# Performance work log

Measured on AMD Instinct MI355X. Metric: run time of the kernel, lower is better.

## Reference

```python
import jax, jax.numpy as jnp
from jax import lax
import numpy as np

P = 0.25  # dropouto


def _lstm(x, Wih, Whh, b):
    """Standard torch-layout LSTM over [B, T, I]; gate order i,f,g,o.
    Wih: [4H, I], Whh: [4H, H], b: [4H] (= b_ih + b_hh). Returns [B, T, H]."""
    B, T, I = x.shape
    H = Whh.shape[1]
    # Precompute input contributions for all timesteps in one GEMM.
    xg = jnp.einsum('bti,gi->btg', x, Wih) + b  # [B, T, 4H]
    xg = jnp.swapaxes(xg, 0, 1)  # [T, B, 4H]

    def step(carry, xt):
        h, c = carry
        g = xt + h @ Whh.T  # [B, 4H]
        i, f, gg, o = jnp.split(g, 4, axis=-1)
        i = jax.nn.sigmoid(i)
        f = jax.nn.sigmoid(f)
        gg = jnp.tanh(gg)
        o = jax.nn.sigmoid(o)
        c = f * c + i * gg
        h = o * jnp.tanh(c)
        return (h, c), h

    h0 = jnp.zeros((B, H), x.dtype)
    c0 = jnp.zeros((B, H), x.dtype)
    _, hs = lax.scan(step, (h0, c0), xg)  # hs: [T, B, H]
    return jnp.swapaxes(hs, 0, 1)


def setup_inputs() -> dict:
    key = jax.random.key(0)
    ks = jax.random.split(key, 10)
    B, T = 512, 4096
    H1, H2 = 16, 1
    s = 0.25  # small init scale
    x = jax.random.normal(ks[0], (B, T, 1), jnp.float32)
    Wih1 = jax.random.normal(ks[1], (4 * H1, 1), jnp.float32) * s
    Whh1 = jax.random.normal(ks[2], (4 * H1, H1), jnp.float32) * s
    b1 = jax.random.normal(ks[3], (4 * H1,), jnp.float32) * s
    Wih2 = jax.random.normal(ks[4], (4 * H2, H1), jnp.float32) * s
    Whh2 = jax.random.normal(ks[5], (4 * H2, H2), jnp.float32) * s
    b2 = jax.random.normal(ks[6], (4 * H2,), jnp.float32) * s
    keep = 1.0 - P
    # Variational dropout masks: one mask per sequence, shared over time.
    mask1 = jax.random.bernoulli(ks[7], keep, (B, 1, H1)).astype(jnp.float32) / keep
    mask2 = jax.random.bernoulli(ks[8], keep, (B, 1, H2)).astype(jnp.float32) / keep
    return {"x": x, "Wih1": Wih1, "Whh1": Whh1, "b1": b1,
            "Wih2": Wih2, "Whh2": Whh2, "b2": b2,
            "mask1": mask1, "mask2": mask2}


def reference(x, Wih1, Whh1, b1, Wih2, Whh2, b2, mask1, mask2):
    out = _lstm(x, Wih1, Whh1, b1) * mask1   # dropouto on lstm1 output
    out = _lstm(out, Wih2, Whh2, b2) * mask2  # dropouto on lstm2 output
    return out  # [B, T, 1]
```

## Files before the change

kernel.cpp:

```cpp
#include <hip/hip_runtime.h>

typedef __fp16 f16x2 __attribute__((ext_vector_type(2)));
typedef unsigned u32x2 __attribute__((ext_vector_type(2)));

static __device__ __forceinline__ float rdlane(float v, int l) {
  return __uint_as_float(__builtin_amdgcn_readlane(__float_as_uint(v), (unsigned)l));
}
static __device__ __forceinline__ unsigned rdlane_u(unsigned v, int l) {
  return __builtin_amdgcn_readlane(v, (unsigned)l);
}

template <int CTRL>
static __device__ __forceinline__ float qperm(float v) {
  return __uint_as_float(__builtin_amdgcn_update_dpp(
      0u, __float_as_uint(v), CTRL, 0xF, 0xF, true));
}

static __device__ __forceinline__ float xswap_hi(float v) {
#if __has_builtin(__builtin_amdgcn_permlane32_swap)
  u32x2 r = __builtin_amdgcn_permlane32_swap(
      __float_as_uint(v), __float_as_uint(v), false, false);
  return __uint_as_float(r.y);
#else
  float a = v, b;
  asm("v_mov_b32 %0, %1\n\t"
      "s_nop 1\n\t"
      "v_permlane32_swap_b32 %1, %0"
      : "=&v"(b), "+v"(a));
  return b;
#endif
}

static __device__ __forceinline__ float exp2a(float x) {
  float r;
  asm("v_exp_f32 %0, %1" : "=v"(r) : "v"(x));
  return r;
}
static __device__ __forceinline__ float rcpa(float x) {
  return __builtin_amdgcn_rcpf(x);
}

static __device__ __forceinline__ float dot2f(f16x2 a, unsigned bu, float c) {
#if __has_builtin(__builtin_amdgcn_fdot2)
  return __builtin_amdgcn_fdot2(a, __builtin_bit_cast(f16x2, bu), c, false);
#else
  float r = c;
  f16x2 b = __builtin_bit_cast(f16x2, bu);
  asm("v_dot2_f32_f16 %0, %1, %2, %0" : "+v"(r) : "v"(a), "v"(b));
  return r;
#endif
}

#define QP_XOR1 0xB1
#define QP_XOR2 0x4E
#define QP_XOR3 0x1B
#define QP_BC3  0xFF

__global__ __launch_bounds__(64, 1) void vdd_lstm_kernel(
    const float* __restrict__ x,
    const float* __restrict__ Wih1,
    const float* __restrict__ Whh1,
    const float* __restrict__ b1,
    const float* __restrict__ Wih2,
    const float* __restrict__ Whh2,
    const float* __restrict__ b2,
    const float* __restrict__ mask1,
    const float* __restrict__ mask2,
    float* __restrict__ out,
    int T) {
  const int b = blockIdx.x;
  const int lane = threadIdx.x;
  const int j = lane >> 2;
  const int gt = lane & 3;
  const int row = gt * 16 + j;

  const float LOG2E = 1.4426950408889634f;
  const bool isg = (gt == 2);
  const float sc = isg ? (-2.f * LOG2E) : (-LOG2E);
  const float aA = isg ? (-4.f * LOG2E) : 1.f;
  const float aC = isg ? (2.f * LOG2E) : 0.f;
  const bool isl1 = (lane == 1);

  f16x2 wh1[8];
#pragma unroll
  for (int m = 0; m < 8; ++m) {
    wh1[m].x = (__fp16)(Whh1[row * 16 + m] * sc);
    wh1[m].y = (__fp16)(Whh1[row * 16 + m + 8] * sc);
  }
  f16x2 wh2[8];
#pragma unroll
  for (int m = 0; m < 8; ++m) {
    wh2[m].x = (__fp16)(Wih2[gt * 16 + m] * mask1[b * 16 + m] * sc);
    wh2[m].y = (__fp16)(Wih2[gt * 16 + m + 8] * mask1[b * 16 + m + 8] * sc);
  }
  const float wih1 = Wih1[row] * sc;
  const float bb1  = b1[row] * sc;
  const float whh2 = Whh2[gt] * sc;
  const float bb2  = b2[gt] * sc;
  const float m2   = mask2[b];

  const float* xb = x + (size_t)b * T;
  float* ob = out + (size_t)b * T;

  float h, cs;
  float cs2p = 0.f;
  float o2p = 0.f;
  float och = 0.f;

  const int NCH = T >> 6;
  const int tmax = T - 1;

  {
    float pre = __fmaf_rn(wih1, xb[0], bb1);
    float a1 = __fmaf_rn(aA, rcpa(1.f + exp2a(pre)), aC);
    float g1 = qperm<QP_XOR2>(a1);
    float o1 = qperm<QP_XOR3>(a1);
    cs = a1 * g1;
    float th = __fmaf_rn(2.f, rcpa(1.f + exp2a(cs)), -1.f);
    h = o1 * th;
  }

  auto body = [&](float sx, bool doSel, int slot) {
    float hhi = xswap_hi(h);
    f16x2 tp = __builtin_bit_cast(
        f16x2, __builtin_amdgcn_cvt_pkrtz(h, hhi));
    unsigned tpu = __builtin_bit_cast(unsigned, tp);
    unsigned sp[8];
#pragma unroll
    for (int m = 0; m < 8; ++m) sp[m] = rdlane_u(tpu, 4 * m);

    float accA = __fmaf_rn(wih1, sx, bb1);
    float accB = dot2f(wh1[1], sp[1], 0.f);
    accA = dot2f(wh1[0], sp[0], accA);
    accB = dot2f(wh1[3], sp[3], accB);
    accA = dot2f(wh1[2], sp[2], accA);
    accB = dot2f(wh1[5], sp[5], accB);
    accA = dot2f(wh1[4], sp[4], accA);
    accB = dot2f(wh1[7], sp[7], accB);
    accA = dot2f(wh1[6], sp[6], accA);
    float pre = accA + accB;

    float accC = dot2f(wh2[0], sp[0], bb2);
    float accD = dot2f(wh2[1], sp[1], 0.f);
    accC = dot2f(wh2[2], sp[2], accC);
    accD = dot2f(wh2[3], sp[3], accD);
    accC = dot2f(wh2[4], sp[4], accC);
    accD = dot2f(wh2[5], sp[5], accD);
    accC = dot2f(wh2[6], sp[6], accC);
    accD = dot2f(wh2[7], sp[7], accD);
    float d2 = accC + accD;

    float a1 = __fmaf_rn(aA, rcpa(1.f + exp2a(pre)), aC);
    float f1 = qperm<QP_XOR1>(a1);
    float g1 = qperm<QP_XOR2>(a1);
    float o1 = qperm<QP_XOR3>(a1);
    cs = __fmaf_rn(f1, cs, a1 * g1);

    float z = isl1 ? cs2p : cs;
    float thv = __fmaf_rn(2.f, rcpa(1.f + exp2a(z)), -1.f);
    float hn = o1 * thv;
    float th2 = rdlane(thv, 1);
    float h2b = o2p * th2;

    float pre2 = __fmaf_rn(whh2, h2b, d2);
    float a2 = __fmaf_rn(aA, rcpa(1.f + exp2a(pre2)), aC);
    float i2l = qperm<QP_XOR1>(a2);
    float g2l = qperm<QP_XOR3>(a2);
    cs2p = __fmaf_rn(a2, cs2p, i2l * g2l);
    o2p = qperm<QP_BC3>(a2);

    float ov = h2b * m2;
    if (doSel) och = (lane == slot) ? ov : och;
    h = hn;
  };

  int idx0 = 2 + lane;
  idx0 = idx0 > tmax ? tmax : idx0;
  float w = xb[idx0];

  body(xb[1], false, 0);

  for (int ch = 0; ch < NCH; ++ch) {
    int idxn = (ch + 1) * 64 + 2 + lane;
    idxn = idxn > tmax ? tmax : idxn;
    float wn = xb[idxn];

#pragma unroll 16
    for (int s2 = 0; s2 < 64; ++s2) {
      float sx = rdlane(w, s2);
      body(sx, true, s2);
    }

    ob[(ch << 6) + lane] = och;
    w = wn;
  }
}

extern "C" void kernel_launch(void* const* d_in, const int* in_sizes, int n_in,
                              void* d_out, int out_size, void* d_ws, size_t ws_size,
                              hipStream_t stream) {
  const float* x     = (const float*)d_in[0];
  const float* Wih1  = (const float*)d_in[1];
  const float* Whh1  = (const float*)d_in[2];
  const float* b1    = (const float*)d_in[3];
  const float* Wih2  = (const float*)d_in[4];
  const float* Whh2  = (const float*)d_in[5];
  const float* b2    = (const float*)d_in[6];
  const float* mask1 = (const float*)d_in[7];
  const float* mask2 = (const float*)d_in[8];
  float* out = (float*)d_out;

  const int B = in_sizes[8];
  const int T = in_sizes[0] / B;

  vdd_lstm_kernel<<<dim3(B), dim3(64), 0, stream>>>(
      x, Wih1, Whh1, b1, Wih2, Whh2, b2, mask1, mask2, out, T);
}
```

Baseline: 540.1 us.

## Split LSTM layers into producer/consumer wavefronts pipelined through LDS

```diff
diff --git a/kernel.cpp b/kernel.cpp
--- a/kernel.cpp
+++ b/kernel.cpp
@@ -56,7 +56,10 @@
 #define QP_XOR3 0x1B
 #define QP_BC3  0xFF
 
-__global__ __launch_bounds__(64, 1) void vdd_lstm_kernel(
+#define SLOT_W 65
+#define BUF_W  (64 * SLOT_W)
+
+__global__ __launch_bounds__(128, 1) void vdd_lstm_kernel(
     const float* __restrict__ x,
     const float* __restrict__ Wih1,
     const float* __restrict__ Whh1,
@@ -68,8 +71,12 @@
     const float* __restrict__ mask2,
     float* __restrict__ out,
     int T) {
+  __shared__ unsigned lds_u[2 * BUF_W];
+
   const int b = blockIdx.x;
-  const int lane = threadIdx.x;
+  const int tid = threadIdx.x;
+  const bool isA = tid < 64;
+  const int lane = tid & 63;
   const int j = lane >> 2;
   const int gt = lane & 3;
   const int row = gt * 16 + j;
@@ -81,118 +88,133 @@
   const float aC = isg ? (2.f * LOG2E) : 0.f;
   const bool isl1 = (lane == 1);
 
-  f16x2 wh1[8];
-#pragma unroll
-  for (int m = 0; m < 8; ++m) {
-    wh1[m].x = (__fp16)(Whh1[row * 16 + m] * sc);
-    wh1[m].y = (__fp16)(Whh1[row * 16 + m + 8] * sc);
-  }
-  f16x2 wh2[8];
-#pragma unroll
-  for (int m = 0; m < 8; ++m) {
-    wh2[m].x = (__fp16)(Wih2[gt * 16 + m] * mask1[b * 16 + m] * sc);
-    wh2[m].y = (__fp16)(Wih2[gt * 16 + m + 8] * mask1[b * 16 + m + 8] * sc);
-  }
-  const float wih1 = Wih1[row] * sc;
-  const float bb1  = b1[row] * sc;
-  const float whh2 = Whh2[gt] * sc;
-  const float bb2  = b2[gt] * sc;
-  const float m2   = mask2[b];
-
   const float* xb = x + (size_t)b * T;
   float* ob = out + (size_t)b * T;
-
-  float h, cs;
-  float cs2p = 0.f;
-  float o2p = 0.f;
-  float och = 0.f;
-
   const int NCH = T >> 6;
   const int tmax = T - 1;
 
-  {
-    float pre = __fmaf_rn(wih1, xb[0], bb1);
-    float a1 = __fmaf_rn(aA, rcpa(1.f + exp2a(pre)), aC);
-    float g1 = qperm<QP_XOR2>(a1);
-    float o1 = qperm<QP_XOR3>(a1);
-    cs = a1 * g1;
-    float th = __fmaf_rn(2.f, rcpa(1.f + exp2a(cs)), -1.f);
-    h = o1 * th;
-  }
-
-  auto body = [&](float sx, bool doSel, int slot) {
-    float hhi = xswap_hi(h);
-    f16x2 tp = __builtin_bit_cast(
-        f16x2, __builtin_amdgcn_cvt_pkrtz(h, hhi));
-    unsigned tpu = __builtin_bit_cast(unsigned, tp);
-    unsigned sp[8];
-#pragma unroll
-    for (int m = 0; m < 8; ++m) sp[m] = rdlane_u(tpu, 4 * m);
-
-    float accA = __fmaf_rn(wih1, sx, bb1);
-    float accB = dot2f(wh1[1], sp[1], 0.f);
-    accA = dot2f(wh1[0], sp[0], accA);
-    accB = dot2f(wh1[3], sp[3], accB);
-    accA = dot2f(wh1[2], sp[2], accA);
-    accB = dot2f(wh1[5], sp[5], accB);
-    accA = dot2f(wh1[4], sp[4], accA);
-    accB = dot2f(wh1[7], sp[7], accB);
-    accA = dot2f(wh1[6], sp[6], accA);
-    float pre = accA + accB;
-
-    float accC = dot2f(wh2[0], sp[0], bb2);
-    float accD = dot2f(wh2[1], sp[1], 0.f);
-    accC = dot2f(wh2[2], sp[2], accC);
-    accD = dot2f(wh2[3], sp[3], accD);
-    accC = dot2f(wh2[4], sp[4], accC);
-    accD = dot2f(wh2[5], sp[5], accD);
-    accC = dot2f(wh2[6], sp[6], accC);
-    accD = dot2f(wh2[7], sp[7], accD);
-    float d2 = accC + accD;
-
-    float a1 = __fmaf_rn(aA, rcpa(1.f + exp2a(pre)), aC);
-    float f1 = qperm<QP_XOR1>(a1);
-    float g1 = qperm<QP_XOR2>(a1);
-    float o1 = qperm<QP_XOR3>(a1);
-    cs = __fmaf_rn(f1, cs, a1 * g1);
-
-    float z = isl1 ? cs2p : cs;
-    float thv = __fmaf_rn(2.f, rcpa(1.f + exp2a(z)), -1.f);
-    float hn = o1 * thv;
-    float th2 = rdlane(thv, 1);
-    float h2b = o2p * th2;
-
-    float pre2 = __fmaf_rn(whh2, h2b, d2);
-    float a2 = __fmaf_rn(aA, rcpa(1.f + exp2a(pre2)), aC);
-    float i2l = qperm<QP_XOR1>(a2);
-    float g2l = qperm<QP_XOR3>(a2);
-    cs2p = __fmaf_rn(a2, cs2p, i2l * g2l);
-    o2p = qperm<QP_BC3>(a2);
-
-    float ov = h2b * m2;
-    if (doSel) och = (lane == slot) ? ov : och;
-    h = hn;
-  };
-
-  int idx0 = 2 + lane;
-  idx0 = idx0 > tmax ? tmax : idx0;
-  float w = xb[idx0];
-
-  body(xb[1], false, 0);
-
-  for (int ch = 0; ch < NCH; ++ch) {
-    int idxn = (ch + 1) * 64 + 2 + lane;
-    idxn = idxn > tmax ? tmax : idxn;
-    float wn = xb[idxn];
+  if (isA) {
+    f16x2 wh1[8];
+#pragma unroll
+    for (int m = 0; m < 8; ++m) {
+      wh1[m].x = (__fp16)(Whh1[row * 16 + m] * sc);
+      wh1[m].y = (__fp16)(Whh1[row * 16 + m + 8] * sc);
+    }
+    const float wih1 = Wih1[row] * sc;
+    const float bb1  = b1[row] * sc;
+
+    float h, cs;
+    {
+      float pre = __fmaf_rn(wih1, xb[0], bb1);
+      float a1 = __fmaf_rn(aA, rcpa(1.f + exp2a(pre)), aC);
+      float g1 = qperm<QP_XOR2>(a1);
+      float o1 = qperm<QP_XOR3>(a1);
+      cs = a1 * g1;
+      float th = __fmaf_rn(2.f, rcpa(1.f + exp2a(cs)), -1.f);
+      h = o1 * th;
+    }
+
+    int idx0 = 1 + lane; idx0 = idx0 > tmax ? tmax : idx0;
+    float w = xb[idx0];
+
+    for (int c = 0; c <= NCH; ++c) {
+      if (c < NCH) {
+        int idxn = (c + 1) * 64 + 1 + lane;
+        idxn = idxn > tmax ? tmax : idxn;
+        float wn = xb[idxn];
+        unsigned* buf = lds_u + (c & 1) * BUF_W;
 
 #pragma unroll 16
-    for (int s2 = 0; s2 < 64; ++s2) {
-      float sx = rdlane(w, s2);
-      body(sx, true, s2);
-    }
-
-    ob[(ch << 6) + lane] = och;
-    w = wn;
+        for (int s = 0; s < 64; ++s) {
+          float hhi = xswap_hi(h);
+          f16x2 tp = __builtin_bit_cast(
+              f16x2, __builtin_amdgcn_cvt_pkrtz(h, hhi));
+          unsigned tpu = __builtin_bit_cast(unsigned, tp);
+          buf[s * SLOT_W + lane] = tpu;
+
+          unsigned sp[8];
+#pragma unroll
+          for (int m = 0; m < 8; ++m) sp[m] = rdlane_u(tpu, 4 * m);
+
+          float sx = rdlane(w, s);
+
+          float accA2 = __fmaf_rn(wih1, sx, bb1);
+          float accB2 = dot2f(wh1[1], sp[1], 0.f);
+          accA2 = dot2f(wh1[0], sp[0], accA2);
+          accB2 = dot2f(wh1[3], sp[3], accB2);
+          accA2 = dot2f(wh1[2], sp[2], accA2);
+          accB2 = dot2f(wh1[5], sp[5], accB2);
+          accA2 = dot2f(wh1[4], sp[4], accA2);
+          accB2 = dot2f(wh1[7], sp[7], accB2);
+          accA2 = dot2f(wh1[6], sp[6], accA2);
+          float pre = accA2 + accB2;
+
+          float a1 = __fmaf_rn(aA, rcpa(1.f + exp2a(pre)), aC);
+          float f1 = qperm<QP_XOR1>(a1);
+          float g1 = qperm<QP_XOR2>(a1);
+          float o1 = qperm<QP_XOR3>(a1);
+          cs = __fmaf_rn(f1, cs, a1 * g1);
+          float th = __fmaf_rn(2.f, rcpa(1.f + exp2a(cs)), -1.f);
+          h = o1 * th;
+        }
+        w = wn;
+      }
+      __syncthreads();
+    }
+  } else {
+    f16x2 wh2[8];
+#pragma unroll
+    for (int m = 0; m < 8; ++m) {
+      wh2[m].x = (__fp16)(Wih2[gt * 16 + m] * mask1[b * 16 + m] * sc);
+      wh2[m].y = (__fp16)(Wih2[gt * 16 + m + 8] * mask1[b * 16 + m + 8] * sc);
+    }
+    const float whh2 = Whh2[gt] * sc;
+    const float bb2  = b2[gt] * sc;
+    const float m2   = mask2[b];
+
+    float cs2p = 0.f;
+    float h2b = 0.f;
+
+    for (int c = 0; c <= NCH; ++c) {
+      if (c > 0) {
+        const int cc = c - 1;
+        const unsigned* buf = lds_u + (cc & 1) * BUF_W;
+        unsigned P[8];
+#pragma unroll
+        for (int m = 0; m < 8; ++m) P[m] = buf[lane * SLOT_W + 4 * m];
+
+        float och = 0.f;
+#pragma unroll 16
+        for (int s = 0; s < 64; ++s) {
+          unsigned sp[8];
+#pragma unroll
+          for (int m = 0; m < 8; ++m) sp[m] = rdlane_u(P[m], s);
+
+          float accC = dot2f(wh2[0], sp[0], bb2);
+          float accD = dot2f(wh2[1], sp[1], 0.f);
+          accC = dot2f(wh2[2], sp[2], accC);
+          accD = dot2f(wh2[3], sp[3], accD);
+          accC = dot2f(wh2[4], sp[4], accC);
+          accD = dot2f(wh2[5], sp[5], accD);
+          accC = dot2f(wh2[6], sp[6], accC);
+          accD = dot2f(wh2[7], sp[7], accD);
+          float pre2 = __fmaf_rn(whh2, h2b, accC + accD);
+
+          float a2 = __fmaf_rn(aA, rcpa(1.f + exp2a(pre2)), aC);
+          float i2l = qperm<QP_XOR1>(a2);
+          float g2l = qperm<QP_XOR3>(a2);
+          cs2p = __fmaf_rn(a2, cs2p, i2l * g2l);
+          float o2b = qperm<QP_BC3>(a2);
+          float thv = __fmaf_rn(2.f, rcpa(1.f + exp2a(cs2p)), -1.f);
+          float th2 = rdlane(thv, 1);
+          h2b = o2b * th2;
+          float ov = h2b * m2;
+          och = (lane == s) ? ov : och;
+        }
+        ob[(cc << 6) + lane] = och;
+      }
+      __syncthreads();
+    }
   }
 }
 
@@ -213,6 +235,6 @@
   const int B = in_sizes[8];
   const int T = in_sizes[0] / B;
 
-  vdd_lstm_kernel<<<dim3(B), dim3(64), 0, stream>>>(
+  vdd_lstm_kernel<<<dim3(B), dim3(128), 0, stream>>>(
       x, Wih1, Whh1, b1, Wih2, Whh2, b2, mask1, mask2, out, T);
 }
```

New measurement: 735.9 us. +36.2%, slower.
